# Performance work log

Measured on AMD Instinct MI355X. Metric: run time of the kernel, lower is better.

## Reference

```python
import jax, jax.numpy as jnp
import numpy as np

N = 8192
IN_F = 256
OUT_F = 64
ALPHA = 0.3  # LeakyReLU negative slope
NEG_INF = -9e15


def setup_inputs() -> dict:
    key = jax.random.key(0)
    k1, k2, k3, k4 = jax.random.split(key, 4)
    h = jax.random.normal(k1, (N, IN_F), dtype=jnp.float32)
    # sparse-ish binary adjacency with self loops (values are 0/1 floats)
    adj = (jax.random.uniform(k2, (N, N)) < 0.05).astype(jnp.float32)
    adj = jnp.maximum(adj, jnp.eye(N, dtype=jnp.float32))
    # xavier_uniform-style scales (gain=1.414)
    w_lim = 1.414 * np.sqrt(6.0 / (IN_F + OUT_F))
    a_lim = 1.414 * np.sqrt(6.0 / (2 * OUT_F + 1))
    W = jax.random.uniform(k3, (IN_F, OUT_F), minval=-w_lim, maxval=w_lim, dtype=jnp.float32)
    a = jax.random.uniform(k4, (2 * OUT_F, 1), minval=-a_lim, maxval=a_lim, dtype=jnp.float32)
    return {"h": h, "adj": adj, "W": W, "a": a}


def reference(h, adj, W, a):
    # Wh: [N, F]
    Wh = h @ W
    # Additive decomposition of the original concat-attention:
    # e_ij = leakyrelu(a[:F].Wh_i + a[F:].Wh_j)  -- identical math, no NxNx2F tensor
    src = Wh @ a[:OUT_F]      # [N, 1]
    dst = Wh @ a[OUT_F:]      # [N, 1]
    e = jax.nn.leaky_relu(src + dst.T, negative_slope=ALPHA)  # [N, N]
    e = e * adj               # faithful: original multiplies by adj before masking
    att = jnp.where(adj > 0, e, NEG_INF)
    att = jax.nn.softmax(att, axis=1)
    # dropout omitted (eval mode / deterministic reference)
    h_prime = att @ Wh        # [N, F]
    return jax.nn.elu(h_prime)
```

## Files before the change

kernel.cpp:

```cpp
#include <hip/hip_runtime.h>
#include <hip/hip_bf16.h>

#define N_NODES 8192
#define IN_F    256
#define OUT_F   64
#define ALPHA   0.3f
#define MBIAS   20.0f
#define CSPL    4
#define COLS_PER (N_NODES / CSPL)
#define NTILES  (COLS_PER / 64)
#define LDP     72

typedef unsigned short u16;
typedef unsigned int   u32;
typedef __attribute__((ext_vector_type(8))) short bf16x8;
typedef __attribute__((ext_vector_type(4))) float f32x4;

__device__ __forceinline__ float bf2f(u32 u) { return __uint_as_float(u << 16); }
__device__ __forceinline__ u32 f2bfbits(float x) {
    u32 u = __float_as_uint(x);
    return (u + 0x7FFFu + ((u >> 16) & 1u)) >> 16;
}
__device__ __forceinline__ float lrelu(float s) { return s > 0.f ? s : ALPHA * s; }

template <bool BF16>
__device__ __forceinline__ float ld(const void* p, size_t idx) {
    if constexpr (BF16) return bf2f(((const u16*)p)[idx]);
    else                return ((const float*)p)[idx];
}

__global__ void gat_detect_kernel(const unsigned* __restrict__ adj_words,
                                  int* __restrict__ flag) {
    *flag = ((adj_words[0] & 0xFFFFu) == 0x3F80u) ? 1 : 0;
}

template <bool BF16>
__device__ __forceinline__ void wh_impl(
    const void* __restrict__ h, const void* __restrict__ W,
    const void* __restrict__ a, float* __restrict__ src,
    float* __restrict__ dst, int i, int lane, float* acc_out)
{
    float acc = 0.f;
#pragma unroll 16
    for (int k = 0; k < IN_F; ++k) {
        float hv = ld<BF16>(h, (size_t)i * IN_F + k);
        float wv = ld<BF16>(W, (size_t)k * OUT_F + lane);
        acc = fmaf(hv, wv, acc);
    }
    float ps = acc * ld<BF16>(a, lane);
    float pd = acc * ld<BF16>(a, OUT_F + lane);
#pragma unroll
    for (int off = 32; off > 0; off >>= 1) {
        ps += __shfl_xor(ps, off, 64);
        pd += __shfl_xor(pd, off, 64);
    }
    if (lane == 0) { src[i] = ps; dst[i] = pd; }
    *acc_out = acc;
}

__global__ __launch_bounds__(256) void gat_wh_kernel(
    const void* __restrict__ h, const void* __restrict__ W,
    const void* __restrict__ a, const int* __restrict__ flag,
    u16* __restrict__ WhT, float* __restrict__ src, float* __restrict__ dst)
{
    __shared__ float accs[4][OUT_F];
    const int tid = threadIdx.x, wave = tid >> 6, lane = tid & 63;
    const int i = blockIdx.x * 4 + wave;
    float acc;
    if (*flag) wh_impl<true >(h, W, a, src, dst, i, lane, &acc);
    else       wh_impl<false>(h, W, a, src, dst, i, lane, &acc);

    accs[wave][lane] = acc;
    __syncthreads();
    if (tid < OUT_F) {
        u32 b0 = f2bfbits(accs[0][tid]);
        u32 b1 = f2bfbits(accs[1][tid]);
        u32 b2 = f2bfbits(accs[2][tid]);
        u32 b3 = f2bfbits(accs[3][tid]);
        uint2 v; v.x = b0 | (b1 << 16); v.y = b2 | (b3 << 16);
        *(uint2*)(WhT + (size_t)tid * N_NODES + blockIdx.x * 4) = v;
    }
}

template <bool BF16>
__device__ __forceinline__ u32 adj_mask16(const void* adjrow_base, int t)
{
    u32 msk = 0;
    if constexpr (BF16) {
        const uint4* p = (const uint4*)((const u16*)adjrow_base + t * 64);
        uint4 a0 = p[0], a1 = p[1];
        u32 aw[8] = {a0.x, a0.y, a0.z, a0.w, a1.x, a1.y, a1.z, a1.w};
#pragma unroll
        for (int e = 0; e < 8; ++e) {
            if (aw[e] & 0xFFFFu) msk |= (1u << (2 * e));
            if (aw[e] >> 16)     msk |= (1u << (2 * e + 1));
        }
    } else {
        const uint4* p = (const uint4*)((const float*)adjrow_base + t * 64);
        uint4 a0 = p[0], a1 = p[1], a2 = p[2], a3 = p[3];
        u32 aw[16] = {a0.x,a0.y,a0.z,a0.w, a1.x,a1.y,a1.z,a1.w,
                      a2.x,a2.y,a2.z,a2.w, a3.x,a3.y,a3.z,a3.w};
#pragma unroll
        for (int e = 0; e < 16; ++e)
            if (aw[e]) msk |= (1u << e);
    }
    return msk;
}

__global__ __launch_bounds__(256) void gat_attn_kernel(
    const void* __restrict__ adj, const u16* __restrict__ WhT,
    const float* __restrict__ src, const float* __restrict__ dst,
    const int* __restrict__ flag,
    float* __restrict__ O_part, float* __restrict__ l_part)
{
    __shared__ alignas(16) u16 Plds[64 * LDP];
    __shared__ alignas(16) u16 Blds[64 * LDP];

    const int tid = threadIdx.x, wave = tid >> 6, lane = tid & 63;
    const int r = tid >> 2, cq = tid & 3;
    const int i0 = blockIdx.x * 64, c0 = blockIdx.y * COLS_PER;
    const int isbf = *flag;

    const float srow = src[i0 + r];
    const float m = lrelu(srow + MBIAS);

    const void* adjrow = isbf
        ? (const void*)((const u16*)adj + (size_t)(i0 + r) * N_NODES + c0 + cq * 16)
        : (const void*)((const float*)adj + (size_t)(i0 + r) * N_NODES + c0 + cq * 16);
    const u16*    whtrow = WhT + (size_t)r * N_NODES + c0 + cq * 16;
    const float4* dstp   = (const float4*)(dst + c0 + cq * 16);

    const int mrow = (lane & 15);
    const int kq   = (lane >> 4) * 8;

    f32x4 acc[4] = {{0,0,0,0},{0,0,0,0},{0,0,0,0},{0,0,0,0}};
    float lacc = 0.f;

    for (int t = 0; t < NTILES; ++t) {
        uint4 b0 = *(const uint4*)(whtrow + t * 64);
        uint4 b1 = *(const uint4*)(whtrow + t * 64 + 8);
        u32 msk = isbf ? adj_mask16<true >(adjrow, t)
                       : adj_mask16<false>(adjrow, t);
        float4 d0 = dstp[t * 16],     d1 = dstp[t * 16 + 1];
        float4 d2 = dstp[t * 16 + 2], d3 = dstp[t * 16 + 3];

        *(uint4*)&Blds[r * LDP + cq * 16]     = b0;
        *(uint4*)&Blds[r * LDP + cq * 16 + 8] = b1;

        u32 po[8];
        {
            float dv[16] = {d0.x,d0.y,d0.z,d0.w, d1.x,d1.y,d1.z,d1.w,
                            d2.x,d2.y,d2.z,d2.w, d3.x,d3.y,d3.z,d3.w};
#pragma unroll
            for (int e = 0; e < 8; ++e) {
                float s0 = lrelu(srow + dv[2 * e]);
                float s1 = lrelu(srow + dv[2 * e + 1]);
                float p0 = (msk & (1u << (2 * e)))     ? __expf(s0 - m) : 0.f;
                float p1 = (msk & (1u << (2 * e + 1))) ? __expf(s1 - m) : 0.f;
                u32 q0 = f2bfbits(p0), q1 = f2bfbits(p1);
                lacc += bf2f(q0) + bf2f(q1);
                po[e] = q0 | (q1 << 16);
            }
        }
        *(uint4*)&Plds[r * LDP + cq * 16]     = *(uint4*)&po[0];
        *(uint4*)&Plds[r * LDP + cq * 16 + 8] = *(uint4*)&po[4];

        __syncthreads();

#pragma unroll
        for (int ks = 0; ks < 2; ++ks) {
            bf16x8 av = *(bf16x8*)&Plds[(16 * wave + mrow) * LDP + ks * 32 + kq];
#pragma unroll
            for (int nt = 0; nt < 4; ++nt) {
                bf16x8 bv = *(bf16x8*)&Blds[(16 * nt + mrow) * LDP + ks * 32 + kq];
                acc[nt] = __builtin_amdgcn_mfma_f32_16x16x32_bf16(av, bv, acc[nt], 0, 0, 0);
            }
        }
        __syncthreads();
    }

    lacc += __shfl_xor(lacc, 1, 64);
    lacc += __shfl_xor(lacc, 2, 64);
    if (cq == 0) l_part[blockIdx.y * N_NODES + i0 + r] = lacc;

    float* Ob = O_part + (size_t)blockIdx.y * N_NODES * OUT_F;
#pragma unroll
    for (int nt = 0; nt < 4; ++nt)
#pragma unroll
        for (int reg = 0; reg < 4; ++reg) {
            int row = i0 + 16 * wave + (lane >> 4) * 4 + reg;
            int col = 16 * nt + (lane & 15);
            Ob[(size_t)row * OUT_F + col] = acc[nt][reg];
        }
}

__global__ __launch_bounds__(256) void gat_reduce_kernel(
    const float* __restrict__ O_part, const float* __restrict__ l_part,
    const int* __restrict__ flag, void* __restrict__ out)
{
    int gid = blockIdx.x * 256 + threadIdx.x;
    int i = gid >> 6;
    float O = 0.f, L = 0.f;
#pragma unroll
    for (int c = 0; c < CSPL; ++c) {
        O += O_part[(size_t)c * N_NODES * OUT_F + gid];
        L += l_part[c * N_NODES + i];
    }
    float hp = O / L;
    float o = hp > 0.f ? hp : expm1f(hp);
    if (*flag) ((u16*)out)[gid] = (u16)f2bfbits(o);
    else       ((float*)out)[gid] = o;
}

extern "C" void kernel_launch(void* const* d_in, const int* in_sizes, int n_in,
                              void* d_out, int out_size, void* d_ws, size_t ws_size,
                              hipStream_t stream)
{
    const void* h   = d_in[0];
    const void* adj = d_in[1];
    const void* W   = d_in[2];
    const void* a   = d_in[3];

    char* ws = (char*)d_ws;
    u16*   WhT    = (u16*)ws;
    float* src    = (float*)(ws + (1u << 20));
    float* dst    = (float*)(ws + (1u << 20) + 32768);
    int*   flag   = (int*)  (ws + (1u << 20) + 65536);
    float* O_part = (float*)(ws + (2u << 20));
    float* l_part = (float*)(ws + (10u << 20));

    gat_detect_kernel<<<1, 1, 0, stream>>>((const unsigned*)adj, flag);
    gat_wh_kernel<<<N_NODES / 4, 256, 0, stream>>>(h, W, a, flag, WhT, src, dst);
    dim3 grid(N_NODES / 64, CSPL);
    gat_attn_kernel<<<grid, 256, 0, stream>>>(adj, WhT, src, dst, flag, O_part, l_part);
    gat_reduce_kernel<<<N_NODES * OUT_F / 256, 256, 0, stream>>>(O_part, l_part, flag, d_out);
}
```

Measured before the change: 437.6 us.

## Double-buffer attention tiles, raise column split, compute four Wh rows per wave

```diff
diff --git a/kernel.cpp b/kernel.cpp
--- a/kernel.cpp
+++ b/kernel.cpp
@@ -6,7 +6,7 @@
 #define OUT_F   64
 #define ALPHA   0.3f
 #define MBIAS   20.0f
-#define CSPL    4
+#define CSPL    8
 #define COLS_PER (N_NODES / CSPL)
 #define NTILES  (COLS_PER / 64)
 #define LDP     72
@@ -35,27 +35,38 @@
 }
 
 template <bool BF16>
-__device__ __forceinline__ void wh_impl(
+__device__ __forceinline__ void wh4_impl(
     const void* __restrict__ h, const void* __restrict__ W,
     const void* __restrict__ a, float* __restrict__ src,
-    float* __restrict__ dst, int i, int lane, float* acc_out)
-{
-    float acc = 0.f;
-#pragma unroll 16
+    float* __restrict__ dst, int i0, int lane, float* accv)
+{
+    float acc0 = 0.f, acc1 = 0.f, acc2 = 0.f, acc3 = 0.f;
+#pragma unroll 8
     for (int k = 0; k < IN_F; ++k) {
-        float hv = ld<BF16>(h, (size_t)i * IN_F + k);
         float wv = ld<BF16>(W, (size_t)k * OUT_F + lane);
-        acc = fmaf(hv, wv, acc);
-    }
-    float ps = acc * ld<BF16>(a, lane);
-    float pd = acc * ld<BF16>(a, OUT_F + lane);
-#pragma unroll
-    for (int off = 32; off > 0; off >>= 1) {
-        ps += __shfl_xor(ps, off, 64);
-        pd += __shfl_xor(pd, off, 64);
-    }
-    if (lane == 0) { src[i] = ps; dst[i] = pd; }
-    *acc_out = acc;
+        float h0 = ld<BF16>(h, (size_t)(i0 + 0) * IN_F + k);
+        float h1 = ld<BF16>(h, (size_t)(i0 + 1) * IN_F + k);
+        float h2 = ld<BF16>(h, (size_t)(i0 + 2) * IN_F + k);
+        float h3 = ld<BF16>(h, (size_t)(i0 + 3) * IN_F + k);
+        acc0 = fmaf(h0, wv, acc0);
+        acc1 = fmaf(h1, wv, acc1);
+        acc2 = fmaf(h2, wv, acc2);
+        acc3 = fmaf(h3, wv, acc3);
+    }
+    float av = ld<BF16>(a, lane);
+    float bv = ld<BF16>(a, OUT_F + lane);
+    float accs[4] = {acc0, acc1, acc2, acc3};
+#pragma unroll
+    for (int r = 0; r < 4; ++r) {
+        float ps = accs[r] * av, pd = accs[r] * bv;
+#pragma unroll
+        for (int off = 32; off > 0; off >>= 1) {
+            ps += __shfl_xor(ps, off, 64);
+            pd += __shfl_xor(pd, off, 64);
+        }
+        if (lane == 0) { src[i0 + r] = ps; dst[i0 + r] = pd; }
+        accv[r] = accs[r];
+    }
 }
 
 __global__ __launch_bounds__(256) void gat_wh_kernel(
@@ -63,22 +74,26 @@
     const void* __restrict__ a, const int* __restrict__ flag,
     u16* __restrict__ WhT, float* __restrict__ src, float* __restrict__ dst)
 {
-    __shared__ float accs[4][OUT_F];
+    __shared__ float accs[16][OUT_F];
     const int tid = threadIdx.x, wave = tid >> 6, lane = tid & 63;
-    const int i = blockIdx.x * 4 + wave;
-    float acc;
-    if (*flag) wh_impl<true >(h, W, a, src, dst, i, lane, &acc);
-    else       wh_impl<false>(h, W, a, src, dst, i, lane, &acc);
-
-    accs[wave][lane] = acc;
+    const int i0 = blockIdx.x * 16 + wave * 4;
+    float av[4];
+    if (*flag) wh4_impl<true >(h, W, a, src, dst, i0, lane, av);
+    else       wh4_impl<false>(h, W, a, src, dst, i0, lane, av);
+#pragma unroll
+    for (int r = 0; r < 4; ++r) accs[wave * 4 + r][lane] = av[r];
     __syncthreads();
     if (tid < OUT_F) {
-        u32 b0 = f2bfbits(accs[0][tid]);
-        u32 b1 = f2bfbits(accs[1][tid]);
-        u32 b2 = f2bfbits(accs[2][tid]);
-        u32 b3 = f2bfbits(accs[3][tid]);
-        uint2 v; v.x = b0 | (b1 << 16); v.y = b2 | (b3 << 16);
-        *(uint2*)(WhT + (size_t)tid * N_NODES + blockIdx.x * 4) = v;
+        u32 w[8];
+#pragma unroll
+        for (int e = 0; e < 8; ++e) {
+            u32 lo = f2bfbits(accs[2 * e][tid]);
+            u32 hi = f2bfbits(accs[2 * e + 1][tid]);
+            w[e] = lo | (hi << 16);
+        }
+        u16* dstp = WhT + (size_t)tid * N_NODES + blockIdx.x * 16;
+        *(uint4*)dstp       = *(uint4*)&w[0];
+        *(uint4*)(dstp + 8) = *(uint4*)&w[4];
     }
 }
 
@@ -107,14 +122,14 @@
     return msk;
 }
 
-__global__ __launch_bounds__(256) void gat_attn_kernel(
+__global__ __launch_bounds__(256, 4) void gat_attn_kernel(
     const void* __restrict__ adj, const u16* __restrict__ WhT,
     const float* __restrict__ src, const float* __restrict__ dst,
     const int* __restrict__ flag,
     float* __restrict__ O_part, float* __restrict__ l_part)
 {
-    __shared__ alignas(16) u16 Plds[64 * LDP];
-    __shared__ alignas(16) u16 Blds[64 * LDP];
+    __shared__ alignas(16) u16 Plds[2][64 * LDP];
+    __shared__ alignas(16) u16 Blds[2][64 * LDP];
 
     const int tid = threadIdx.x, wave = tid >> 6, lane = tid & 63;
     const int r = tid >> 2, cq = tid & 3;
@@ -132,52 +147,68 @@
 
     const int mrow = (lane & 15);
     const int kq   = (lane >> 4) * 8;
+    const int pw   = r * LDP + cq * 16;
 
     f32x4 acc[4] = {{0,0,0,0},{0,0,0,0},{0,0,0,0},{0,0,0,0}};
     float lacc = 0.f;
 
+    uint4  pb0, pb1;
+    u32    pmsk;
+    float4 pd0, pd1, pd2, pd3;
+
+#define LOAD_TILE(t)                                                      \
+    do {                                                                  \
+        pb0 = *(const uint4*)(whtrow + (t) * 64);                         \
+        pb1 = *(const uint4*)(whtrow + (t) * 64 + 8);                     \
+        pmsk = isbf ? adj_mask16<true >(adjrow, (t))                      \
+                    : adj_mask16<false>(adjrow, (t));                     \
+        pd0 = dstp[(t) * 16];     pd1 = dstp[(t) * 16 + 1];               \
+        pd2 = dstp[(t) * 16 + 2]; pd3 = dstp[(t) * 16 + 3];               \
+    } while (0)
+
+#define STAGE_TILE(buf)                                                   \
+    do {                                                                  \
+        *(uint4*)&Blds[buf][pw]     = pb0;                                \
+        *(uint4*)&Blds[buf][pw + 8] = pb1;                                \
+        float dv[16] = {pd0.x,pd0.y,pd0.z,pd0.w, pd1.x,pd1.y,pd1.z,pd1.w, \
+                        pd2.x,pd2.y,pd2.z,pd2.w, pd3.x,pd3.y,pd3.z,pd3.w};\
+        u32 po[8];                                                        \
+        _Pragma("unroll")                                                 \
+        for (int e = 0; e < 8; ++e) {                                     \
+            float s0 = lrelu(srow + dv[2 * e]);                           \
+            float s1 = lrelu(srow + dv[2 * e + 1]);                       \
+            float p0 = (pmsk & (1u << (2 * e)))     ? __expf(s0 - m) : 0.f;\
+            float p1 = (pmsk & (1u << (2 * e + 1))) ? __expf(s1 - m) : 0.f;\
+            u32 q0 = f2bfbits(p0), q1 = f2bfbits(p1);                     \
+            lacc += bf2f(q0) + bf2f(q1);            \
+            po[e] = q0 | (q1 << 16);                                      \
+        }                                                                 \
+        *(uint4*)&Plds[buf][pw]     = *(uint4*)&po[0];                    \
+        *(uint4*)&Plds[buf][pw + 8] = *(uint4*)&po[4];                    \
+    } while (0)
+
+    LOAD_TILE(0);
+    STAGE_TILE(0);
+    __syncthreads();
+
     for (int t = 0; t < NTILES; ++t) {
-        uint4 b0 = *(const uint4*)(whtrow + t * 64);
-        uint4 b1 = *(const uint4*)(whtrow + t * 64 + 8);
-        u32 msk = isbf ? adj_mask16<true >(adjrow, t)
-                       : adj_mask16<false>(adjrow, t);
-        float4 d0 = dstp[t * 16],     d1 = dstp[t * 16 + 1];
-        float4 d2 = dstp[t * 16 + 2], d3 = dstp[t * 16 + 3];
-
-        *(uint4*)&Blds[r * LDP + cq * 16]     = b0;
-        *(uint4*)&Blds[r * LDP + cq * 16 + 8] = b1;
-
-        u32 po[8];
-        {
-            float dv[16] = {d0.x,d0.y,d0.z,d0.w, d1.x,d1.y,d1.z,d1.w,
-                            d2.x,d2.y,d2.z,d2.w, d3.x,d3.y,d3.z,d3.w};
-#pragma unroll
-            for (int e = 0; e < 8; ++e) {
-                float s0 = lrelu(srow + dv[2 * e]);
-                float s1 = lrelu(srow + dv[2 * e + 1]);
-                float p0 = (msk & (1u << (2 * e)))     ? __expf(s0 - m) : 0.f;
-                float p1 = (msk & (1u << (2 * e + 1))) ? __expf(s1 - m) : 0.f;
-                u32 q0 = f2bfbits(p0), q1 = f2bfbits(p1);
-                lacc += bf2f(q0) + bf2f(q1);
-                po[e] = q0 | (q1 << 16);
+        const int cur = t & 1, nxt = cur ^ 1;
+        if (t + 1 < NTILES) LOAD_TILE(t + 1);
+
+#pragma unroll
+        for (int ks = 0; ks < 2; ++ks) {
+            bf16x8 avf = *(bf16x8*)&Plds[cur][(16 * wave + mrow) * LDP + ks * 32 + kq];
+#pragma unroll
+            for (int nt = 0; nt < 4; ++nt) {
+                bf16x8 bvf = *(bf16x8*)&Blds[cur][(16 * nt + mrow) * LDP + ks * 32 + kq];
+                acc[nt] = __builtin_amdgcn_mfma_f32_16x16x32_bf16(avf, bvf, acc[nt], 0, 0, 0);
             }
         }
-        *(uint4*)&Plds[r * LDP + cq * 16]     = *(uint4*)&po[0];
-        *(uint4*)&Plds[r * LDP + cq * 16 + 8] = *(uint4*)&po[4];
-
+        if (t + 1 < NTILES) STAGE_TILE(nxt);
         __syncthreads();
-
-#pragma unroll
-        for (int ks = 0; ks < 2; ++ks) {
-            bf16x8 av = *(bf16x8*)&Plds[(16 * wave + mrow) * LDP + ks * 32 + kq];
-#pragma unroll
-            for (int nt = 0; nt < 4; ++nt) {
-                bf16x8 bv = *(bf16x8*)&Blds[(16 * nt + mrow) * LDP + ks * 32 + kq];
-                acc[nt] = __builtin_amdgcn_mfma_f32_16x16x32_bf16(av, bv, acc[nt], 0, 0, 0);
-            }
-        }
-        __syncthreads();
-    }
+    }
+#undef LOAD_TILE
+#undef STAGE_TILE
 
     lacc += __shfl_xor(lacc, 1, 64);
     lacc += __shfl_xor(lacc, 2, 64);
@@ -227,10 +258,10 @@
     float* dst    = (float*)(ws + (1u << 20) + 32768);
     int*   flag   = (int*)  (ws + (1u << 20) + 65536);
     float* O_part = (float*)(ws + (2u << 20));
-    float* l_part = (float*)(ws + (10u << 20));
+    float* l_part = (float*)(ws + (18u << 20));
 
     gat_detect_kernel<<<1, 1, 0, stream>>>((const unsigned*)adj, flag);
-    gat_wh_kernel<<<N_NODES / 4, 256, 0, stream>>>(h, W, a, flag, WhT, src, dst);
+    gat_wh_kernel<<<N_NODES / 16, 256, 0, stream>>>(h, W, a, flag, WhT, src, dst);
     dim3 grid(N_NODES / 64, CSPL);
     gat_attn_kernel<<<grid, 256, 0, stream>>>(adj, WhT, src, dst, flag, O_part, l_part);
     gat_reduce_kernel<<<N_NODES * OUT_F / 256, 256, 0, stream>>>(O_part, l_part, flag, d_out);
```

After: 442.2 us. About the same (+1.1%).
